# Kernel tuning notes

Hardware: AMD Instinct MI355X
Metric: run time of the kernel (lower is better)

## Reference

```python
import jax, jax.numpy as jnp
import numpy as np

EMBED_DIM = 1024
NUM_HEADS = 16
HEAD_DIM = EMBED_DIM // NUM_HEADS
B, T = 8, 1024


def setup_inputs() -> dict:
    key = jax.random.key(0)
    ks = jax.random.split(key, 8)
    s = EMBED_DIM ** -0.5
    return {
        "query": jax.random.normal(ks[0], (B, T, EMBED_DIM), jnp.float32),
        "key": jax.random.normal(ks[1], (B, T, EMBED_DIM), jnp.float32),
        "value": jax.random.normal(ks[2], (B, T, EMBED_DIM), jnp.float32),
        "key_padding_mask": jnp.zeros((B, T), dtype=bool),
        "attn_mask": jax.random.normal(ks[3], (T, T), jnp.float32) * 0.02,
        "in_proj_weight": jax.random.normal(ks[4], (3 * EMBED_DIM, EMBED_DIM), jnp.float32) * s,
        "in_proj_bias": jax.random.normal(ks[5], (3 * EMBED_DIM,), jnp.float32) * 0.02,
        "out_proj_weight": jax.random.normal(ks[6], (EMBED_DIM, EMBED_DIM), jnp.float32) * s,
        "out_proj_bias": jax.random.normal(ks[7], (EMBED_DIM,), jnp.float32) * 0.02,
    }


def reference(query, key, value, key_padding_mask, attn_mask,
              in_proj_weight, in_proj_bias, out_proj_weight, out_proj_bias):
    E, H, Dh = EMBED_DIM, NUM_HEADS, HEAD_DIM
    scale = Dh ** -0.5
    w_q, w_k, w_v = in_proj_weight[:E], in_proj_weight[E:2 * E], in_proj_weight[2 * E:]
    b_q, b_k, b_v = in_proj_bias[:E], in_proj_bias[E:2 * E], in_proj_bias[2 * E:]

    b, t_q, _ = query.shape
    t_k = key.shape[1]
    # projections: F.linear(x, W, b) = x @ W.T + b
    q = (query @ w_q.T + b_q).reshape(b, t_q, H, Dh).transpose(0, 2, 1, 3)
    k = (key @ w_k.T + b_k).reshape(b, t_k, H, Dh).transpose(0, 2, 1, 3)
    v = (value @ w_v.T + b_v).reshape(b, t_k, H, Dh).transpose(0, 2, 1, 3)

    scores = jnp.einsum('bhqd,bhkd->bhqk', q, k) * scale  # [B,H,Tq,Tk]
    scores = jnp.where(key_padding_mask[:, None, None, :], -jnp.inf, scores)
    scores = scores + attn_mask  # broadcast [Tq,Tk] over batch/heads
    attn = jax.nn.softmax(scores, axis=-1)
    out = jnp.einsum('bhqk,bhkd->bhqd', attn, v)
    out = out.transpose(0, 2, 1, 3).reshape(b, t_q, E)
    return out @ out_proj_weight.T + out_proj_bias
```

## Files before the change

### kernel.cpp

```cpp
#include <hip/hip_runtime.h>
#include <cstdint>
#include <cstddef>

#define E_DIM   1024
#define NHEADS  16
#define DHEAD   64
#define BATCH   8
#define SEQ     1024
#define MROWS   (BATCH*SEQ)

#define LOG2E 1.44269504f

typedef __bf16 bf16;
typedef __attribute__((ext_vector_type(8))) __bf16 bf16x8;
typedef __attribute__((ext_vector_type(4))) __bf16 bf16x4;
typedef __attribute__((ext_vector_type(4))) float f32x4;

typedef const __attribute__((address_space(1))) unsigned int gu32;
typedef __attribute__((address_space(3))) unsigned int lu32;

__global__ __launch_bounds__(256)
void split_kernel(const float* __restrict__ src, bf16* __restrict__ hi,
                  bf16* __restrict__ lo, int n4)
{
    int i = blockIdx.x * 256 + threadIdx.x;
    if (i >= n4) return;
    float4 x = ((const float4*)src)[i];
    bf16x4 h, l;
    h[0] = (bf16)x.x; l[0] = (bf16)(x.x - (float)h[0]);
    h[1] = (bf16)x.y; l[1] = (bf16)(x.y - (float)h[1]);
    h[2] = (bf16)x.z; l[2] = (bf16)(x.z - (float)h[2]);
    h[3] = (bf16)x.w; l[3] = (bf16)(x.w - (float)h[3]);
    ((bf16x4*)hi)[i] = h;
    ((bf16x4*)lo)[i] = l;
}

__global__ __launch_bounds__(256)
void scale_f32_kernel(const float* __restrict__ src, float* __restrict__ dst,
                      float scale, int n4)
{
    int i = blockIdx.x * 256 + threadIdx.x;
    if (i >= n4) return;
    float4 x = ((const float4*)src)[i];
    x.x *= scale; x.y *= scale; x.z *= scale; x.w *= scale;
    ((float4*)dst)[i] = x;
}

__global__ __launch_bounds__(512)
void gemm_nt_mfma(const bf16* __restrict__ Ahi, const bf16* __restrict__ Alo,
                  const bf16* __restrict__ Whi, const bf16* __restrict__ Wlo,
                  const float* __restrict__ bias,
                  float* __restrict__ outF, bf16* __restrict__ outHi,
                  int M, int N, int K, int mode)
{
    __shared__ bf16 Ahs[2][128 * 32];
    __shared__ bf16 Als[2][128 * 32];
    __shared__ bf16 Whs[2][128 * 32];
    __shared__ bf16 Wls[2][128 * 32];

    const int tid  = threadIdx.x;
    const int lane = tid & 63;
    const int wid  = tid >> 6;
    const int wm = (wid >> 1) * 32;
    const int wn = (wid & 1) * 64;
    const int fr = lane & 15;
    const int fk = (lane >> 4) * 8;

    const int mBase = blockIdx.y * 128;
    const int nBase = blockIdx.x * 128;

    const int rowA0 = tid >> 2;
    const int colA0 = (tid & 3) * 8;

    const int dcol = lane & 15;
    float bv[4];
#pragma unroll
    for (int bn = 0; bn < 4; ++bn)
        bv[bn] = bias[nBase + wn + bn * 16 + dcol];

    f32x4 acc[2][4];
#pragma unroll
    for (int i = 0; i < 2; ++i)
#pragma unroll
        for (int j = 0; j < 4; ++j) acc[i][j] = (f32x4){0.f, 0.f, 0.f, 0.f};

    auto stage = [&](int k0, int bi) {
        const size_t ga0 = (size_t)(mBase + rowA0) * K + k0 + colA0;
        const size_t gw0 = (size_t)(nBase + rowA0) * K + k0 + colA0;
        __builtin_amdgcn_global_load_lds((gu32*)(Ahi + ga0), (lu32*)&Ahs[bi][wid * 512], 16, 0, 0);
        __builtin_amdgcn_global_load_lds((gu32*)(Alo + ga0), (lu32*)&Als[bi][wid * 512], 16, 0, 0);
        __builtin_amdgcn_global_load_lds((gu32*)(Whi + gw0), (lu32*)&Whs[bi][wid * 512], 16, 0, 0);
        __builtin_amdgcn_global_load_lds((gu32*)(Wlo + gw0), (lu32*)&Wls[bi][wid * 512], 16, 0, 0);
    };

    stage(0, 0);

    const int NIT = K >> 5;
#pragma unroll 1
    for (int it = 0; it < NIT; ++it) {
        const int cur = it & 1;
        if (it + 1 < NIT) {
            stage((it + 1) << 5, cur ^ 1);
            asm volatile("s_waitcnt vmcnt(4)" ::: "memory");
        } else {
            asm volatile("s_waitcnt vmcnt(0)" ::: "memory");
        }
        __builtin_amdgcn_s_barrier();

        const bf16* As = Ahs[cur];
        const bf16* Al = Als[cur];
        const bf16* Ws = Whs[cur];
        const bf16* Wl = Wls[cur];

        bf16x8 afh[2], afl[2], bfh[4], bfl[4];
#pragma unroll
        for (int am = 0; am < 2; ++am) {
            afh[am] = *(const bf16x8*)&As[(wm + am * 16 + fr) * 32 + fk];
            afl[am] = *(const bf16x8*)&Al[(wm + am * 16 + fr) * 32 + fk];
        }
#pragma unroll
        for (int bn = 0; bn < 4; ++bn) {
            bfh[bn] = *(const bf16x8*)&Ws[(wn + bn * 16 + fr) * 32 + fk];
            bfl[bn] = *(const bf16x8*)&Wl[(wn + bn * 16 + fr) * 32 + fk];
        }
#pragma unroll
        for (int am = 0; am < 2; ++am)
#pragma unroll
            for (int bn = 0; bn < 4; ++bn) {
                acc[am][bn] = __builtin_amdgcn_mfma_f32_16x16x32_bf16(afh[am], bfh[bn], acc[am][bn], 0, 0, 0);
                acc[am][bn] = __builtin_amdgcn_mfma_f32_16x16x32_bf16(afh[am], bfl[bn], acc[am][bn], 0, 0, 0);
                acc[am][bn] = __builtin_amdgcn_mfma_f32_16x16x32_bf16(afl[am], bfh[bn], acc[am][bn], 0, 0, 0);
            }
        __builtin_amdgcn_s_barrier();
    }

    const int drow = (lane >> 4) * 4;
#pragma unroll
    for (int bn = 0; bn < 4; ++bn) {
        const int col = nBase + wn + bn * 16 + dcol;
#pragma unroll
        for (int am = 0; am < 2; ++am) {
#pragma unroll
            for (int r = 0; r < 4; ++r) {
                const int row = mBase + wm + am * 16 + drow + r;
                const float v = acc[am][bn][r] + bv[bn];
                if (mode == 0) {
                    outF[(size_t)row * N + col] = v;
                } else {
                    const int b = row >> 10, t = row & 1023;
                    const int h = col >> 6,  d = col & 63;
                    size_t idx;
                    if (mode == 1)
                        idx = (((size_t)(b * NHEADS + h)) * SEQ + t) * DHEAD + d;
                    else
                        idx = (((size_t)(b * NHEADS + h)) * DHEAD + d) * SEQ + t;
                    outHi[idx] = (bf16)v;
                }
            }
        }
    }
}

__global__ __launch_bounds__(256)
void attn_mfma_kernel(const bf16* __restrict__ qkv,
                      const float* __restrict__ mask_f,
                      const unsigned char* __restrict__ kpad,
                      bf16* __restrict__ ctx_hi, bf16* __restrict__ ctx_lo)
{
    __shared__ bf16 Ks [2][4096];
    __shared__ bf16 Vts[2][4096];
    __shared__ bf16 Pn[4][1024];

    const int tid  = threadIdx.x;
    const int lane = tid & 63;
    const int wid  = tid >> 6;
    const int c16  = lane & 15;
    const int quad = lane >> 4;

    const int bh = blockIdx.x;
    const int qt = blockIdx.y;
    const int b = bh >> 4, h = bh & 15;

    const size_t seg = (size_t)MROWS * E_DIM;
    const size_t headoff = (size_t)bh * SEQ * DHEAD;
    const bf16* Q_g  = qkv + headoff;
    const bf16* K_g  = qkv + seg + headoff;
    const bf16* Vt_g = qkv + 2 * seg + headoff;

    const int qglob = qt * 64 + wid * 16 + c16;

    bf16x8 qf[2];
#pragma unroll
    for (int ks = 0; ks < 2; ++ks)
        qf[ks] = *(const bf16x8*)&Q_g[(size_t)qglob * DHEAD + quad * 8 + ks * 32];

    float m_i = -1e30f, l_i = 0.f;
    f32x4 oacc[4];
#pragma unroll
    for (int dt = 0; dt < 4; ++dt) oacc[dt] = (f32x4){0.f, 0.f, 0.f, 0.f};

    const int row0 = tid >> 3,         c0 = (tid & 7) ^ (row0 & 7);
    const int row1 = (tid + 256) >> 3, c1 = ((tid + 256) & 7) ^ (row1 & 7);

    auto stage = [&](int kt, int bi) {
        const int ktb = kt * 64;
        const size_t k0 = (size_t)(ktb + row0) * DHEAD + c0 * 8;
        const size_t k1 = (size_t)(ktb + row1) * DHEAD + c1 * 8;
        const size_t v0 = (size_t)row0 * SEQ + ktb + c0 * 8;
        const size_t v1 = (size_t)row1 * SEQ + ktb + c1 * 8;
        __builtin_amdgcn_global_load_lds((gu32*)(K_g + k0),  (lu32*)&Ks [bi][wid * 512],        16, 0, 0);
        __builtin_amdgcn_global_load_lds((gu32*)(K_g + k1),  (lu32*)&Ks [bi][2048 + wid * 512], 16, 0, 0);
        __builtin_amdgcn_global_load_lds((gu32*)(Vt_g + v0), (lu32*)&Vts[bi][wid * 512],        16, 0, 0);
        __builtin_amdgcn_global_load_lds((gu32*)(Vt_g + v1), (lu32*)&Vts[bi][2048 + wid * 512], 16, 0, 0);
    };

    stage(0, 0);
    __syncthreads();

    const int pxor = (c16 & 7) << 3;
    const size_t kpb = (size_t)b * SEQ + quad * 4;

#pragma unroll 1
    for (int kt = 0; kt < 16; ++kt) {
        const int cur = kt & 1;
        const int ktb = kt * 64;

        float4 mvf[4];
        unsigned kpu[4];
#pragma unroll
        for (int st = 0; st < 4; ++st) {
            mvf[st] = *(const float4*)&mask_f[(size_t)qglob * SEQ + ktb + st * 16 + quad * 4];
            kpu[st] = *(const unsigned*)&kpad[kpb + ktb + st * 16];
        }

        if (kt < 15) stage(kt + 1, cur ^ 1);

        f32x4 sacc[4];
#pragma unroll
        for (int st = 0; st < 4; ++st) sacc[st] = (f32x4){0.f, 0.f, 0.f, 0.f};
#pragma unroll
        for (int st = 0; st < 4; ++st) {
            const int row = st * 16 + c16;
            const int sw  = row & 7;
#pragma unroll
            for (int ks = 0; ks < 2; ++ks) {
                const int cp = ((quad + ks * 4) ^ sw);
                bf16x8 kh = *(const bf16x8*)&Ks[cur][(row * 8 + cp) * 8];
                sacc[st] = __builtin_amdgcn_mfma_f32_16x16x32_bf16(kh, qf[ks], sacc[st], 0, 0, 0);
            }
        }

        float s[16];
#pragma unroll
        for (int st = 0; st < 4; ++st) {
#pragma unroll
            for (int r = 0; r < 4; ++r) {
                const float mv = (r == 0) ? mvf[st].x : (r == 1) ? mvf[st].y
                               : (r == 2) ? mvf[st].z : mvf[st].w;
                s[st * 4 + r] = fmaf(sacc[st][r], 0.125f * LOG2E, mv);
            }
        }
        if (__any((kpu[0] | kpu[1] | kpu[2] | kpu[3]) != 0u)) {
#pragma unroll
            for (int st = 0; st < 4; ++st)
#pragma unroll
                for (int r = 0; r < 4; ++r)
                    if ((kpu[st] >> (r * 8)) & 0xff) s[st * 4 + r] = -2e30f;
        }
        float t8[8];
#pragma unroll
        for (int i = 0; i < 8; ++i) t8[i] = fmaxf(s[i], s[i + 8]);
#pragma unroll
        for (int i = 0; i < 4; ++i) t8[i] = fmaxf(t8[i], t8[i + 4]);
        float tm = fmaxf(fmaxf(t8[0], t8[1]), fmaxf(t8[2], t8[3]));
        tm = fmaxf(tm, __shfl_xor(tm, 16, 64));
        tm = fmaxf(tm, __shfl_xor(tm, 32, 64));

        if (!__all(tm <= m_i + 11.5416f)) {
            const float mnew  = fmaxf(m_i, tm);
            const float alpha = __builtin_amdgcn_exp2f(m_i - mnew);
            l_i *= alpha;
#pragma unroll
            for (int dt = 0; dt < 4; ++dt)
#pragma unroll
                for (int r = 0; r < 4; ++r) oacc[dt][r] *= alpha;
            m_i = mnew;
        }

        float p[16];
#pragma unroll
        for (int i = 0; i < 16; ++i) p[i] = __builtin_amdgcn_exp2f(s[i] - m_i);
        float u8[8];
#pragma unroll
        for (int i = 0; i < 8; ++i) u8[i] = p[i] + p[i + 8];
#pragma unroll
        for (int i = 0; i < 4; ++i) u8[i] += u8[i + 4];
        float ps = (u8[0] + u8[1]) + (u8[2] + u8[3]);
        ps += __shfl_xor(ps, 16, 64);
        ps += __shfl_xor(ps, 32, 64);
        l_i += ps;

#pragma unroll
        for (int st = 0; st < 4; ++st) {
            bf16x4 ph;
#pragma unroll
            for (int r = 0; r < 4; ++r) ph[r] = (bf16)p[st * 4 + r];
            *(bf16x4*)&Pn[wid][c16 * 64 + ((st * 16 + quad * 4) ^ pxor)] = ph;
        }
        bf16x8 pf[2];
#pragma unroll
        for (int ks = 0; ks < 2; ++ks)
            pf[ks] = *(const bf16x8*)&Pn[wid][c16 * 64 + ((ks * 32 + quad * 8) ^ pxor)];

#pragma unroll
        for (int dt = 0; dt < 4; ++dt) {
            const int row = dt * 16 + c16;
            const int sw  = row & 7;
#pragma unroll
            for (int ks = 0; ks < 2; ++ks) {
                const int cp = ((quad + ks * 4) ^ sw);
                bf16x8 vh = *(const bf16x8*)&Vts[cur][(row * 8 + cp) * 8];
                oacc[dt] = __builtin_amdgcn_mfma_f32_16x16x32_bf16(vh, pf[ks], oacc[dt], 0, 0, 0);
            }
        }

        __syncthreads();
    }

    const float invl = 1.0f / l_i;
#pragma unroll
    for (int dt = 0; dt < 4; ++dt) {
        bf16x4 oh, ol;
#pragma unroll
        for (int r = 0; r < 4; ++r) {
            float v = oacc[dt][r] * invl;
            oh[r] = (bf16)v;
            ol[r] = (bf16)(v - (float)oh[r]);
        }
        size_t idx = ((size_t)b * SEQ + qglob) * E_DIM + h * DHEAD + dt * 16 + quad * 4;
        *(bf16x4*)&ctx_hi[idx] = oh;
        *(bf16x4*)&ctx_lo[idx] = ol;
    }
}

extern "C" void kernel_launch(void* const* d_in, const int* in_sizes, int n_in,
                              void* d_out, int out_size, void* d_ws, size_t ws_size,
                              hipStream_t stream)
{
    const float* inputs[3] = { (const float*)d_in[0], (const float*)d_in[1],
                               (const float*)d_in[2] };
    const unsigned char* kpad = (const unsigned char*)d_in[3];
    const float* attn_mask = (const float*)d_in[4];
    const float* w_in  = (const float*)d_in[5];
    const float* b_in  = (const float*)d_in[6];
    const float* w_out = (const float*)d_in[7];
    const float* b_out = (const float*)d_in[8];
    float* out = (float*)d_out;

    char* ws = (char*)d_ws;
    const size_t MB = 1024 * 1024;
    bf16*  bufA_hi  = (bf16*)(ws + 0 * MB);
    bf16*  bufA_lo  = (bf16*)(ws + 16 * MB);
    bf16*  w_in_hi  = (bf16*)(ws + 32 * MB);
    bf16*  w_in_lo  = (bf16*)(ws + 38 * MB);
    bf16*  w_out_hi = (bf16*)(ws + 44 * MB);
    bf16*  w_out_lo = (bf16*)(ws + 46 * MB);
    bf16*  qkv      = (bf16*)(ws + 48 * MB);
    float* mask_f   = (float*)(ws + 96 * MB);
    bf16*  ctx_hi   = (bf16*)(ws + 0 * MB);
    bf16*  ctx_lo   = (bf16*)(ws + 16 * MB);

    const size_t seg = (size_t)MROWS * E_DIM;

    split_kernel<<<(3 * E_DIM * E_DIM / 4 + 255) / 256, 256, 0, stream>>>(
        w_in, w_in_hi, w_in_lo, 3 * E_DIM * E_DIM / 4);
    split_kernel<<<(E_DIM * E_DIM / 4 + 255) / 256, 256, 0, stream>>>(
        w_out, w_out_hi, w_out_lo, E_DIM * E_DIM / 4);
    scale_f32_kernel<<<(SEQ * SEQ / 4 + 255) / 256, 256, 0, stream>>>(
        attn_mask, mask_f, LOG2E, SEQ * SEQ / 4);

    for (int z = 0; z < 3; ++z) {
        split_kernel<<<(int)(seg / 4 / 256), 256, 0, stream>>>(
            inputs[z], bufA_hi, bufA_lo, (int)(seg / 4));
        gemm_nt_mfma<<<dim3(E_DIM / 128, MROWS / 128), 512, 0, stream>>>(
            bufA_hi, bufA_lo,
            w_in_hi + (size_t)z * E_DIM * E_DIM, w_in_lo + (size_t)z * E_DIM * E_DIM,
            b_in + z * E_DIM,
            nullptr, qkv + (size_t)z * seg,
            MROWS, E_DIM, E_DIM, (z == 2) ? 2 : 1);
    }

    attn_mfma_kernel<<<dim3(BATCH * NHEADS, SEQ / 64), 256, 0, stream>>>(
        qkv, mask_f, kpad, ctx_hi, ctx_lo);

    gemm_nt_mfma<<<dim3(E_DIM / 128, MROWS / 128), 512, 0, stream>>>(
        ctx_hi, ctx_lo, w_out_hi, w_out_lo, b_out,
        out, nullptr, MROWS, E_DIM, E_DIM, 0);
}
```

Baseline: 514.1 us.

## Swizzle GEMM LDS layout, raise MFMA wave priority, store attn mask as bf16

Three separate changes. The GEMM's LDS staging gets an XOR-style rotation of the 8-element column chunks, applied on both the global-to-LDS store and the fragment reads, to cut LDS bank conflicts. s_setprio(1) is wrapped around the MFMA blocks in the GEMM and attention kernels so those waves get issue priority. The pre-scaled attention mask is stored as bf16 instead of fp32, which halves mask traffic in the attention loop but loses some mask precision.

```diff
diff --git a/kernel.cpp b/kernel.cpp
--- a/kernel.cpp
+++ b/kernel.cpp
@@ -36,14 +36,16 @@
 }
 
 __global__ __launch_bounds__(256)
-void scale_f32_kernel(const float* __restrict__ src, float* __restrict__ dst,
-                      float scale, int n4)
+void cvt_bf16_kernel(const float* __restrict__ src, bf16* __restrict__ dst,
+                     float scale, int n4)
 {
     int i = blockIdx.x * 256 + threadIdx.x;
     if (i >= n4) return;
     float4 x = ((const float4*)src)[i];
-    x.x *= scale; x.y *= scale; x.z *= scale; x.w *= scale;
-    ((float4*)dst)[i] = x;
+    bf16x4 h;
+    h[0] = (bf16)(x.x * scale); h[1] = (bf16)(x.y * scale);
+    h[2] = (bf16)(x.z * scale); h[3] = (bf16)(x.w * scale);
+    ((bf16x4*)dst)[i] = h;
 }
 
 __global__ __launch_bounds__(512)
@@ -64,13 +66,14 @@
     const int wm = (wid >> 1) * 32;
     const int wn = (wid & 1) * 64;
     const int fr = lane & 15;
-    const int fk = (lane >> 4) * 8;
+    const int fq = lane >> 4;
+    const int fk = ((fq + (fr >> 1)) & 3) * 8;
 
     const int mBase = blockIdx.y * 128;
     const int nBase = blockIdx.x * 128;
 
     const int rowA0 = tid >> 2;
-    const int colA0 = (tid & 3) * 8;
+    const int colA0 = (((tid & 3) - ((tid >> 3) & 3)) & 3) * 8;
 
     const int dcol = lane & 15;
     float bv[4];
@@ -123,6 +126,7 @@
             bfh[bn] = *(const bf16x8*)&Ws[(wn + bn * 16 + fr) * 32 + fk];
             bfl[bn] = *(const bf16x8*)&Wl[(wn + bn * 16 + fr) * 32 + fk];
         }
+        __builtin_amdgcn_s_setprio(1);
 #pragma unroll
         for (int am = 0; am < 2; ++am)
 #pragma unroll
@@ -131,6 +135,7 @@
                 acc[am][bn] = __builtin_amdgcn_mfma_f32_16x16x32_bf16(afh[am], bfl[bn], acc[am][bn], 0, 0, 0);
                 acc[am][bn] = __builtin_amdgcn_mfma_f32_16x16x32_bf16(afl[am], bfh[bn], acc[am][bn], 0, 0, 0);
             }
+        __builtin_amdgcn_s_setprio(0);
         __builtin_amdgcn_s_barrier();
     }
 
@@ -163,7 +168,7 @@
 
 __global__ __launch_bounds__(256)
 void attn_mfma_kernel(const bf16* __restrict__ qkv,
-                      const float* __restrict__ mask_f,
+                      const bf16* __restrict__ mask_bf,
                       const unsigned char* __restrict__ kpad,
                       bf16* __restrict__ ctx_hi, bf16* __restrict__ ctx_lo)
 {
@@ -225,11 +230,11 @@
         const int cur = kt & 1;
         const int ktb = kt * 64;
 
-        float4 mvf[4];
+        bf16x4 mvh[4];
         unsigned kpu[4];
 #pragma unroll
         for (int st = 0; st < 4; ++st) {
-            mvf[st] = *(const float4*)&mask_f[(size_t)qglob * SEQ + ktb + st * 16 + quad * 4];
+            mvh[st] = *(const bf16x4*)&mask_bf[(size_t)qglob * SEQ + ktb + st * 16 + quad * 4];
             kpu[st] = *(const unsigned*)&kpad[kpb + ktb + st * 16];
         }
 
@@ -238,6 +243,7 @@
         f32x4 sacc[4];
 #pragma unroll
         for (int st = 0; st < 4; ++st) sacc[st] = (f32x4){0.f, 0.f, 0.f, 0.f};
+        __builtin_amdgcn_s_setprio(1);
 #pragma unroll
         for (int st = 0; st < 4; ++st) {
             const int row = st * 16 + c16;
@@ -249,16 +255,14 @@
                 sacc[st] = __builtin_amdgcn_mfma_f32_16x16x32_bf16(kh, qf[ks], sacc[st], 0, 0, 0);
             }
         }
+        __builtin_amdgcn_s_setprio(0);
 
         float s[16];
 #pragma unroll
         for (int st = 0; st < 4; ++st) {
 #pragma unroll
-            for (int r = 0; r < 4; ++r) {
-                const float mv = (r == 0) ? mvf[st].x : (r == 1) ? mvf[st].y
-                               : (r == 2) ? mvf[st].z : mvf[st].w;
-                s[st * 4 + r] = fmaf(sacc[st][r], 0.125f * LOG2E, mv);
-            }
+            for (int r = 0; r < 4; ++r)
+                s[st * 4 + r] = fmaf(sacc[st][r], 0.125f * LOG2E, (float)mvh[st][r]);
         }
         if (__any((kpu[0] | kpu[1] | kpu[2] | kpu[3]) != 0u)) {
 #pragma unroll
@@ -312,6 +316,7 @@
         for (int ks = 0; ks < 2; ++ks)
             pf[ks] = *(const bf16x8*)&Pn[wid][c16 * 64 + ((ks * 32 + quad * 8) ^ pxor)];
 
+        __builtin_amdgcn_s_setprio(1);
 #pragma unroll
         for (int dt = 0; dt < 4; ++dt) {
             const int row = dt * 16 + c16;
@@ -323,6 +328,7 @@
                 oacc[dt] = __builtin_amdgcn_mfma_f32_16x16x32_bf16(vh, pf[ks], oacc[dt], 0, 0, 0);
             }
         }
+        __builtin_amdgcn_s_setprio(0);
 
         __syncthreads();
     }
@@ -359,16 +365,16 @@
 
     char* ws = (char*)d_ws;
     const size_t MB = 1024 * 1024;
-    bf16*  bufA_hi  = (bf16*)(ws + 0 * MB);
-    bf16*  bufA_lo  = (bf16*)(ws + 16 * MB);
-    bf16*  w_in_hi  = (bf16*)(ws + 32 * MB);
-    bf16*  w_in_lo  = (bf16*)(ws + 38 * MB);
-    bf16*  w_out_hi = (bf16*)(ws + 44 * MB);
-    bf16*  w_out_lo = (bf16*)(ws + 46 * MB);
-    bf16*  qkv      = (bf16*)(ws + 48 * MB);
-    float* mask_f   = (float*)(ws + 96 * MB);
-    bf16*  ctx_hi   = (bf16*)(ws + 0 * MB);
-    bf16*  ctx_lo   = (bf16*)(ws + 16 * MB);
+    bf16* bufA_hi  = (bf16*)(ws + 0 * MB);
+    bf16* bufA_lo  = (bf16*)(ws + 16 * MB);
+    bf16* w_in_hi  = (bf16*)(ws + 32 * MB);
+    bf16* w_in_lo  = (bf16*)(ws + 38 * MB);
+    bf16* w_out_hi = (bf16*)(ws + 44 * MB);
+    bf16* w_out_lo = (bf16*)(ws + 46 * MB);
+    bf16* qkv      = (bf16*)(ws + 48 * MB);
+    bf16* mask_bf  = (bf16*)(ws + 96 * MB);
+    bf16* ctx_hi   = (bf16*)(ws + 0 * MB);
+    bf16* ctx_lo   = (bf16*)(ws + 16 * MB);
 
     const size_t seg = (size_t)MROWS * E_DIM;
 
@@ -376,8 +382,8 @@
         w_in, w_in_hi, w_in_lo, 3 * E_DIM * E_DIM / 4);
     split_kernel<<<(E_DIM * E_DIM / 4 + 255) / 256, 256, 0, stream>>>(
         w_out, w_out_hi, w_out_lo, E_DIM * E_DIM / 4);
-    scale_f32_kernel<<<(SEQ * SEQ / 4 + 255) / 256, 256, 0, stream>>>(
-        attn_mask, mask_f, LOG2E, SEQ * SEQ / 4);
+    cvt_bf16_kernel<<<(SEQ * SEQ / 4 + 255) / 256, 256, 0, stream>>>(
+        attn_mask, mask_bf, LOG2E, SEQ * SEQ / 4);
 
     for (int z = 0; z < 3; ++z) {
         split_kernel<<<(int)(seg / 4 / 256), 256, 0, stream>>>(
@@ -391,7 +397,7 @@
     }
 
     attn_mfma_kernel<<<dim3(BATCH * NHEADS, SEQ / 64), 256, 0, stream>>>(
-        qkv, mask_f, kpad, ctx_hi, ctx_lo);
+        qkv, mask_bf, kpad, ctx_hi, ctx_lo);
 
     gemm_nt_mfma<<<dim3(E_DIM / 128, MROWS / 128), 512, 0, stream>>>(
         ctx_hi, ctx_lo, w_out_hi, w_out_lo, b_out,
```

Result: no change. 508.3 us (-1.1%).
